# Optimization experiments

Measured on AMD Instinct MI355X. Metric: run time of the kernel, lower is better.

The kernel has to match this reference:

```python
import jax, jax.numpy as jnp
import numpy as np

H, HD, C = 16, 64, 64            # num_heads, head_dim, mini_batch_size
BASE_LR = 1.0
EPS = 1e-6                        # ttt LN eps (ln_fwd / ln_fused_l2_bwd)


def _l2norm(x):
    return x / jnp.maximum(jnp.linalg.norm(x, axis=-1, keepdims=True), 1e-12)


def _ln_fwd(x, g, b):
    mu = x.mean(-1, keepdims=True)
    var = x.var(-1, keepdims=True)
    return g * ((x - mu) * jax.lax.rsqrt(var + EPS)) + b


def _ln_l2_bwd(x, tgt, g, b):
    # gradient of ||LN(x)*g+b - tgt||^2 / 2 wrt x
    D = x.shape[-1]
    mu = x.mean(-1, keepdims=True)
    var = x.var(-1, keepdims=True)
    std = jnp.sqrt(var + EPS)
    xh = (x - mu) / std
    gout = (g * xh + b) - tgt
    gxh = gout * g
    return (D * gxh - gxh.sum(-1, keepdims=True) - xh * (gxh * xh).sum(-1, keepdims=True)) / (D * std)


def setup_inputs() -> dict:
    key = jax.random.key(0)
    ks = jax.random.split(key, 12)
    B, L, D = 4, 8192, 1024
    std = 0.02
    return {
        'hidden_states': jax.random.normal(ks[0], (B, L, D), jnp.float32),
        'wq_w': jax.random.normal(ks[1], (D, D), jnp.float32) * std,
        'wq_b': jnp.zeros((D,), jnp.float32),
        'wk_w': jax.random.normal(ks[2], (D, D), jnp.float32) * std,
        'wk_b': jnp.zeros((D,), jnp.float32),
        'wv_w': jax.random.normal(ks[3], (D, D), jnp.float32) * std,
        'wv_b': jnp.zeros((D,), jnp.float32),
        'wo_w': jax.random.normal(ks[4], (D, D), jnp.float32) * std,
        'wo_b': jnp.zeros((D,), jnp.float32),
        'ttt_norm_weight': jnp.ones((H, HD), jnp.float32),
        'ttt_norm_bias': jnp.zeros((H, HD), jnp.float32),
        'ttt_lr_weight': jax.random.normal(ks[5], (H, 1, D), jnp.float32) * std,
        'ttt_lr_bias': jnp.zeros((H, 1), jnp.float32),
        'W1': jax.random.normal(ks[6], (H, HD, HD), jnp.float32) * std,
        'b1': jnp.zeros((H, 1, HD), jnp.float32),
        'post_norm_w': jnp.ones((D,), jnp.float32),
        'post_norm_b': jnp.zeros((D,), jnp.float32),
    }


def _forward(hidden_states, wq_w, wq_b, wk_w, wk_b, wv_w, wv_b, wo_w, wo_b,
             ttt_norm_weight, ttt_norm_bias, ttt_lr_weight, ttt_lr_bias,
             W1, b1, post_norm_w, post_norm_b):
    B, L, D = hidden_states.shape
    NC = L // C
    XQ = (hidden_states @ wq_w.T + wq_b).reshape(B, L, H, HD)
    XK = (hidden_states @ wk_w.T + wk_b).reshape(B, L, H, HD)
    XV = (hidden_states @ wv_w.T + wv_b).reshape(B, L, H, HD)
    XQ = _l2norm(XQ)
    XK = _l2norm(XK)
    # ln_reconstruction_target (uses sample std, ddof=1, eps=1e-5 on std)
    d = XV - XK
    mu = d.mean(-1, keepdims=True)
    sd = d.std(-1, keepdims=True, ddof=1)
    XV = ttt_norm_weight[None, None] * ((d - mu) / (sd + 1e-5)) + ttt_norm_bias[None, None] + XK
    # reshape to mini-batches: [B,H,NC,C,HD]
    Xmb = hidden_states.reshape(B, NC, C, D)
    to_mb = lambda t: t.transpose(0, 2, 1, 3).reshape(B, H, NC, C, HD)
    XQ, XK, XV = to_mb(XQ), to_mb(XK), to_mb(XV)
    # eta: sigmoid lr gate per token, row-broadcast over mini-batch
    ttt_lr = jax.nn.sigmoid(jnp.einsum('bnkc,hdc->bhnkd', Xmb, ttt_lr_weight)
                            + ttt_lr_bias.reshape(1, H, 1, 1, 1))     # [B,H,NC,C,1]
    eta = jnp.swapaxes(ttt_lr, -1, -2) * (BASE_LR / HD / C)           # [B,H,NC,1,C]
    mask = jnp.tril(jnp.ones((C, C), hidden_states.dtype))
    g = ttt_norm_weight[None, :, None, :]
    bta = ttt_norm_bias[None, :, None, :]
    W0 = jnp.broadcast_to(W1[None], (B, H, HD, HD))
    b0 = jnp.broadcast_to(b1[None], (B, H, 1, HD))

    def step(carry, xs):
        W, bvec = carry
        xq, xk, xv, eta_row = xs                      # eta_row: [B,H,1,C]
        Z1 = xk @ W + bvec                            # [B,H,C,HD]
        grad = _ln_l2_bwd(Z1, xv - xk, g, bta)        # [B,H,C,HD]
        Attn = mask * jnp.einsum('bhid,bhjd->bhij', xq, xk)   # [B,H,C,C]
        eta_full = jnp.broadcast_to(eta_row, Attn.shape)      # [B,H,C,C]
        b1_bar = bvec - (mask * eta_full) @ grad              # [B,H,C,HD]
        Z1_bar = xq @ W - (eta_full * Attn) @ grad + b1_bar
        last_eta = eta_full[..., -1, :, None]                 # [B,H,C,1]
        W_new = W - jnp.einsum('bhcd,bhce->bhde', last_eta * xk, grad)
        b_new = bvec - (last_eta * grad).sum(-2, keepdims=True)
        out = xq + _ln_fwd(Z1_bar, g, bta)
        return (W_new, b_new), out

    xs = (jnp.moveaxis(XQ, 2, 0), jnp.moveaxis(XK, 2, 0),
          jnp.moveaxis(XV, 2, 0), jnp.moveaxis(eta, 2, 0))
    _, outs = jax.lax.scan(step, (W0, b0), xs)        # outs: [NC,B,H,C,HD]
    y = jnp.moveaxis(outs, 0, 2).reshape(B, H, L, HD).transpose(0, 2, 1, 3).reshape(B, L, D)
    # post LayerNorm (eps=1e-6) + output projection
    mu2 = y.mean(-1, keepdims=True)
    var2 = y.var(-1, keepdims=True)
    y = post_norm_w * ((y - mu2) * jax.lax.rsqrt(var2 + 1e-6)) + post_norm_b
    return y @ wo_w.T + wo_b


def reference(hidden_states, wq_w, wq_b, wk_w, wk_b, wv_w, wv_b, wo_w, wo_b,
              ttt_norm_weight, ttt_norm_bias, ttt_lr_weight, ttt_lr_bias,
              W1, b1, post_norm_w, post_norm_b):
    return _forward(hidden_states, wq_w, wq_b, wk_w, wk_b, wv_w, wv_b, wo_w, wo_b,
                    ttt_norm_weight, ttt_norm_bias, ttt_lr_weight, ttt_lr_bias,
                    W1, b1, post_norm_w, post_norm_b)
```

## Files before the change

kernel.cpp:

```cpp
#include <hip/hip_runtime.h>


typedef __attribute__((ext_vector_type(8))) short short8;
typedef __attribute__((ext_vector_type(4))) float f32x4;
typedef __attribute__((ext_vector_type(4))) unsigned short us4;

__device__ __forceinline__ float bf2f(unsigned short s) {
  union { unsigned int u; float f; } c;
  c.u = ((unsigned int)s) << 16;
  return c.f;
}
__device__ __forceinline__ unsigned short f2bf(float f) {
  union { float f; unsigned int u; } c;
  c.f = f;
  unsigned int u = c.u;
  return (unsigned short)((u + 0x7FFFu + ((u >> 16) & 1u)) >> 16);
}

__device__ __forceinline__ void gload_lds16(const void* g, void* l) {
  __builtin_amdgcn_global_load_lds(
      (const __attribute__((address_space(1))) unsigned int*)g,
      (__attribute__((address_space(3))) unsigned int*)l, 16, 0, 0);
}

__device__ __forceinline__ float dpp16_sum(float x) {
  int v = __float_as_int(x);
  x += __int_as_float(__builtin_amdgcn_update_dpp(v, v, 0xB1, 0xF, 0xF, true));
  v = __float_as_int(x);
  x += __int_as_float(__builtin_amdgcn_update_dpp(v, v, 0x4E, 0xF, 0xF, true));
  v = __float_as_int(x);
  x += __int_as_float(__builtin_amdgcn_update_dpp(v, v, 0x141, 0xF, 0xF, true));
  v = __float_as_int(x);
  x += __int_as_float(__builtin_amdgcn_update_dpp(v, v, 0x140, 0xF, 0xF, true));
  return x;
}

__device__ __forceinline__ void barrier_fast() {
  __builtin_amdgcn_sched_barrier(0);
  asm volatile("s_waitcnt lgkmcnt(0)" ::: "memory");
  __builtin_amdgcn_s_barrier();
  asm volatile("" ::: "memory");
  __builtin_amdgcn_sched_barrier(0);
}
__device__ __forceinline__ void bar_nowait() {
  __builtin_amdgcn_sched_barrier(0);
  asm volatile("" ::: "memory");
  __builtin_amdgcn_s_barrier();
  asm volatile("" ::: "memory");
  __builtin_amdgcn_sched_barrier(0);
}

__global__ __launch_bounds__(256) void cvt_f32_bf16(
    const float* __restrict__ in, unsigned short* __restrict__ out, long n) {
  long i = ((long)blockIdx.x * 256 + threadIdx.x) * 4;
  if (i + 3 < n) {
    float4 v = *(const float4*)&in[i];
    us4 o = { f2bf(v.x), f2bf(v.y), f2bf(v.z), f2bf(v.w) };
    *(us4*)&out[i] = o;
  }
}

__global__ __launch_bounds__(256) void build_wcat(
    const float* __restrict__ wq, const float* __restrict__ wk,
    const float* __restrict__ wv, const float* __restrict__ lrw,
    const float* __restrict__ wqb, const float* __restrict__ wkb,
    const float* __restrict__ wvb, const float* __restrict__ lrb,
    unsigned short* __restrict__ Wcat, float* __restrict__ biasc) {
  int i = blockIdx.x * 256 + threadIdx.x;
  int row = i >> 10, col = i & 1023;
  float v;
  if (row < 1024)      v = wq[i];
  else if (row < 2048) v = wk[i - 1048576];
  else if (row < 3072) v = wv[i - 2097152];
  else if (row < 3088) v = lrw[(row - 3072) * 1024 + col];
  else                 v = 0.f;
  Wcat[i] = f2bf(v);
  if (i < 3328) {
    float bv;
    if (i < 1024)      bv = wqb[i];
    else if (i < 2048) bv = wkb[i - 1024];
    else if (i < 3072) bv = wvb[i - 2048];
    else if (i < 3088) bv = lrb[i - 3072];
    else               bv = 0.f;
    biasc[i] = bv;
  }
}

template <int WRITE_BF16>
__global__ __launch_bounds__(512, 1) void gemm256(
    const unsigned short* __restrict__ A, const unsigned short* __restrict__ B,
    const float* __restrict__ bias, void* __restrict__ Cout,
    long M, long N, long K, int NTILN, long ldc) {
  __shared__ __align__(16) unsigned short g_lds[65536];
  char* ldsc = (char*)g_lds;
  const int tid = threadIdx.x, lane = tid & 63, wid = tid >> 6;
  const int wm = wid >> 2, wn = wid & 3;
  const int l15 = lane & 15, lg = lane >> 4;

  unsigned nwg = gridDim.x, bid = blockIdx.x;
  unsigned cpx = nwg >> 3;
  unsigned swz = (bid & 7) * cpx + (bid >> 3);
  unsigned nidx = swz % (unsigned)NTILN, midx = swz / (unsigned)NTILN;
  const long m0 = (long)midx * 256, n0 = (long)nidx * 256;
  const long ldab = K * 2;

  const int srow = wid * 16 + (lane >> 2);
  const int scol = ((lane & 3) * 16) ^ (((lane >> 3) & 3) << 4);
  const int sdst = wid * 1024;
  const char* Ab = (const char*)A;
  const char* Bb = (const char*)B;

  const int acol = (lg * 16) ^ (((l15 >> 1) & 3) << 4);
  const int aro = (wm * 128 + l15) * 64 + acol;
  const int bro = 65536 + (wn * 64 + l15) * 64 + acol;

#define STG_A(tt, h, bb)                                                     \
  gload_lds16(Ab + (size_t)(m0 + (h) * 128 + srow) * ldab + (size_t)(tt) * 64 \
                  + scol,                                                     \
              ldsc + (bb) * 16384 + (h) * 8192 + sdst)
#define STG_B(tt, h, bb)                                                     \
  gload_lds16(Bb + (size_t)(n0 + (h) * 128 + srow) * ldab + (size_t)(tt) * 64 \
                  + scol,                                                     \
              ldsc + 65536 + (bb) * 16384 + (h) * 8192 + sdst)

  f32x4 acc[8][4];
#pragma unroll
  for (int m = 0; m < 8; ++m)
#pragma unroll
    for (int n = 0; n < 4; ++n) acc[m][n] = (f32x4){0.f, 0.f, 0.f, 0.f};

  const int NT = (int)(K >> 5);

#pragma unroll
  for (int tt = 0; tt < 3; ++tt) {
    STG_A(tt, 0, tt); STG_A(tt, 1, tt);
    STG_B(tt, 0, tt); STG_B(tt, 1, tt);
  }
  asm volatile("s_waitcnt vmcnt(8)" ::: "memory");
  bar_nowait();

#pragma unroll 1
  for (int t = 0; t < NT; ++t) {
    const int buf = t & 3, sb = (t + 3) & 3;
    const bool doStage = (t + 3 < NT);
    const char* ab = ldsc + buf * 16384 + aro;
    const char* bb = ldsc + buf * 16384 + bro;

    short8 av[4], bv[4];
#pragma unroll
    for (int i = 0; i < 4; ++i) av[i] = *(const short8*)(ab + i * 1024);
#pragma unroll
    for (int nf = 0; nf < 4; ++nf) bv[nf] = *(const short8*)(bb + nf * 1024);
    if (doStage) { STG_A(t + 3, 0, sb); STG_A(t + 3, 1, sb); }
    bar_nowait();
    __builtin_amdgcn_s_setprio(1);
#pragma unroll
    for (int i = 0; i < 4; ++i)
#pragma unroll
      for (int nf = 0; nf < 4; ++nf)
        acc[i][nf] = __builtin_amdgcn_mfma_f32_16x16x32_bf16(av[i], bv[nf],
                                                             acc[i][nf], 0, 0, 0);
    __builtin_amdgcn_s_setprio(0);
    bar_nowait();

#pragma unroll
    for (int i = 0; i < 4; ++i) av[i] = *(const short8*)(ab + 4096 + i * 1024);
    if (doStage) { STG_B(t + 3, 0, sb); STG_B(t + 3, 1, sb); }
    bar_nowait();
    __builtin_amdgcn_s_setprio(1);
#pragma unroll
    for (int i = 0; i < 4; ++i)
#pragma unroll
      for (int nf = 0; nf < 4; ++nf)
        acc[4 + i][nf] = __builtin_amdgcn_mfma_f32_16x16x32_bf16(
            av[i], bv[nf], acc[4 + i][nf], 0, 0, 0);
    __builtin_amdgcn_s_setprio(0);
    asm volatile("s_waitcnt vmcnt(8)" ::: "memory");
    bar_nowait();
  }
#undef STG_A
#undef STG_B

#pragma unroll
  for (int mf = 0; mf < 8; ++mf) {
    long r0 = m0 + wm * 128 + mf * 16 + lg * 4;
#pragma unroll
    for (int nf = 0; nf < 4; ++nf) {
      long c = n0 + wn * 64 + nf * 16 + l15;
      float bvv = bias ? bias[c] : 0.f;
#pragma unroll
      for (int j = 0; j < 4; ++j) {
        float v = acc[mf][nf][j] + bvv;
        if (WRITE_BF16)
          ((unsigned short*)Cout)[(r0 + j) * ldc + c] = f2bf(v);
        else
          ((float*)Cout)[(r0 + j) * ldc + c] = v;
      }
    }
  }
}

__global__ __launch_bounds__(256) void stage2(
    const unsigned short* __restrict__ QKVL, const float* __restrict__ tnw,
    const float* __restrict__ tnb, unsigned short* __restrict__ XQn,
    unsigned short* __restrict__ XKn, unsigned short* __restrict__ TGT,
    float* __restrict__ eta_buf) {
  int wid = threadIdx.x >> 6, lane = threadIdx.x & 63;
  long idx = (long)blockIdx.x * 4 + wid;
  long t = idx >> 4;
  int h = (int)(idx & 15);
  size_t base = (size_t)t * 3328;
  float q = bf2f(QKVL[base + h * 64 + lane]);
  float k = bf2f(QKVL[base + 1024 + h * 64 + lane]);
  float v = bf2f(QKVL[base + 2048 + h * 64 + lane]);
  float sq = q * q, sk = k * k;
#pragma unroll
  for (int o = 1; o < 64; o <<= 1) {
    sq += __shfl_xor(sq, o);
    sk += __shfl_xor(sk, o);
  }
  float qn = q / fmaxf(sqrtf(sq), 1e-12f);
  float kn = k / fmaxf(sqrtf(sk), 1e-12f);
  float d = v - kn;
  float s1 = d, s2 = d * d;
#pragma unroll
  for (int o = 1; o < 64; o <<= 1) {
    s1 += __shfl_xor(s1, o);
    s2 += __shfl_xor(s2, o);
  }
  float mu = s1 * 0.015625f;
  float var1 = fmaxf(s2 - 64.f * mu * mu, 0.f) * (1.f / 63.f);
  float sd = sqrtf(var1);
  float tgt = tnw[h * 64 + lane] * ((d - mu) / (sd + 1e-5f)) + tnb[h * 64 + lane];
  size_t ob = (size_t)t * 1024 + h * 64 + lane;
  XQn[ob] = f2bf(qn);
  XKn[ob] = f2bf(kn);
  TGT[ob] = f2bf(tgt);
  if (lane == 0) {
    float logit = bf2f(QKVL[base + 3072 + h]);
    float sig = 1.f / (1.f + expf(-logit));
    long bb = t >> 13, l = t & 8191;
    eta_buf[(size_t)(bb * 16 + h) * 8192 + l] = sig * (1.f / 4096.f);
  }
}

__global__ __launch_bounds__(512, 1) void ttt_scan(
    const unsigned short* __restrict__ XQ, const unsigned short* __restrict__ XK,
    const unsigned short* __restrict__ TG, const float* __restrict__ eta_buf,
    const float* __restrict__ W1, const float* __restrict__ b1,
    const float* __restrict__ tnw, const float* __restrict__ tnb,
    float* __restrict__ y) {
  const int bh = blockIdx.x;
  const int b = bh >> 4, h = bh & 15;
  const int tid = threadIdx.x;
  const int lane = tid & 63, wid = tid >> 6;
  const bool isA = wid < 4;
  const int q = wid & 3;
  const int l15 = lane & 15, lg = lane >> 4;

  __shared__ __align__(16) unsigned short xq_s[2][64 * 72];
  __shared__ __align__(16) unsigned short tg_s[2][64 * 72];
  __shared__ __align__(16) unsigned short xk_s[2][64 * 72];
  __shared__ __align__(16) unsigned short gc_s[64 * 72];
  __shared__ __align__(16) unsigned short gradT[64 * 72];
  __shared__ __align__(16) unsigned short xkTe[64 * 72];
  __shared__ __align__(16) unsigned short WT_b[2][64 * 72];
  __shared__ float eta_s[2][64];
  __shared__ float bpart[4][64];

  const size_t tokb = (size_t)b * 8192;
  const int col0 = h * 64;
  const int rr_ = q * 16 + (lane >> 3);
  const int c8_ = (lane & 7) * 8;

  short8 pA0[2], pA1[2], pB0[2];
  float peta = 0.f;
  float bstv[4], gwv[4], gbv[4];
  f32x4 Wreg[4];

  if (isA) {
#pragma unroll
    for (int n = 0; n < 4; ++n) {
      int e = n * 16 + l15;
      bstv[n] = b1[h * 64 + e];
      gwv[n] = tnw[h * 64 + e];
      gbv[n] = tnb[h * 64 + e];
    }
#pragma unroll
    for (int j = 0; j < 2; ++j) {
      size_t g = (tokb + rr_ + j * 8) * 1024 + col0 + c8_;
      pA0[j] = *(const short8*)&XQ[g];
      pA1[j] = *(const short8*)&TG[g];
    }
#pragma unroll
    for (int j = 0; j < 2; ++j) {
      int rr = rr_ + j * 8;
      *(short8*)&xq_s[0][rr * 72 + c8_] = pA0[j];
      *(short8*)&tg_s[0][rr * 72 + c8_] = pA1[j];
    }
#pragma unroll
    for (int j = 0; j < 2; ++j) {
      size_t g = (tokb + 64 + rr_ + j * 8) * 1024 + col0 + c8_;
      pA0[j] = *(const short8*)&XQ[g];
      pA1[j] = *(const short8*)&TG[g];
    }
  } else {
#pragma unroll
    for (int j = 0; j < 2; ++j)
      pB0[j] = *(const short8*)&XK[(tokb + rr_ + j * 8) * 1024 + col0 + c8_];
#pragma unroll
    for (int j = 0; j < 2; ++j)
      *(short8*)&xk_s[0][(rr_ + j * 8) * 72 + c8_] = pB0[j];
#pragma unroll
    for (int j = 0; j < 2; ++j)
      pB0[j] = *(const short8*)&XK[(tokb + 64 + rr_ + j * 8) * 1024 + col0 + c8_];
#pragma unroll
    for (int n = 0; n < 4; ++n)
#pragma unroll
      for (int jj = 0; jj < 4; ++jj) {
        int d = q * 16 + lg * 4 + jj, e = n * 16 + l15;
        float w = W1[h * 4096 + d * 64 + e];
        Wreg[n][jj] = w;
        WT_b[0][e * 72 + d] = f2bf(w);
      }
    if (wid == 4) {
      eta_s[0][lane] = eta_buf[(size_t)bh * 8192 + lane];
      peta = eta_buf[(size_t)bh * 8192 + 64 + lane];
    }
  }
  __syncthreads();

  for (int nc = 0; nc < 128; ++nc) {
    const int p = nc & 1;
    const unsigned short* WTc = WT_b[p];
    unsigned short* WTn = WT_b[p ^ 1];

    if (isA) {
      if (nc) {
#pragma unroll
        for (int n = 0; n < 4; ++n) {
          int e = n * 16 + l15;
          bstv[n] -= bpart[0][e] + bpart[1][e] + bpart[2][e] + bpart[3][e];
        }
      }
      if (nc + 1 < 128) {
#pragma unroll
        for (int j = 0; j < 2; ++j) {
          int rr = rr_ + j * 8;
          *(short8*)&xq_s[p ^ 1][rr * 72 + c8_] = pA0[j];
          *(short8*)&tg_s[p ^ 1][rr * 72 + c8_] = pA1[j];
        }
      }
      if (nc + 2 < 128) {
#pragma unroll
        for (int j = 0; j < 2; ++j) {
          size_t g = (tokb + (nc + 2) * 64 + rr_ + j * 8) * 1024 + col0 + c8_;
          pA0[j] = *(const short8*)&XQ[g];
          pA1[j] = *(const short8*)&TG[g];
        }
      }
      f32x4 accZ[4];
#pragma unroll
      for (int n = 0; n < 4; ++n)
        accZ[n] = (f32x4){bstv[n], bstv[n], bstv[n], bstv[n]};
      __builtin_amdgcn_s_setprio(1);
#pragma unroll
      for (int kk = 0; kk < 2; ++kk) {
        const int ko = kk * 32 + lg * 8;
        short8 a_xk = *(const short8*)&xk_s[p][(q * 16 + l15) * 72 + ko];
#pragma unroll
        for (int n = 0; n < 4; ++n) {
          short8 b_w = *(const short8*)&WTc[(n * 16 + l15) * 72 + ko];
          accZ[n] = __builtin_amdgcn_mfma_f32_16x16x32_bf16(a_xk, b_w, accZ[n], 0, 0, 0);
        }
      }
      __builtin_amdgcn_s_setprio(0);
      float grv[4][4];
#pragma unroll
      for (int j = 0; j < 4; ++j) {
        const int r = q * 16 + lg * 4 + j;
        float z[4], s1 = 0.f, s2 = 0.f;
#pragma unroll
        for (int n = 0; n < 4; ++n) {
          z[n] = accZ[n][j];
          s1 += z[n];
          s2 += z[n] * z[n];
        }
        s1 = dpp16_sum(s1);
        s2 = dpp16_sum(s2);
        float mu = s1 * 0.015625f;
        float var = s2 * 0.015625f - mu * mu;
        float rstd = rsqrtf(var + 1e-6f);
        float xh[4], gx[4], s3 = 0.f, s4 = 0.f;
#pragma unroll
        for (int n = 0; n < 4; ++n) {
          xh[n] = (z[n] - mu) * rstd;
          float tg = bf2f(tg_s[p][r * 72 + n * 16 + l15]);
          float go = gwv[n] * xh[n] + gbv[n] - tg;
          gx[n] = go * gwv[n];
          s3 += gx[n];
          s4 += gx[n] * xh[n];
        }
        s3 = dpp16_sum(s3);
        s4 = dpp16_sum(s4);
#pragma unroll
        for (int n = 0; n < 4; ++n)
          grv[n][j] = (64.f * gx[n] - s3 - xh[n] * s4) * rstd * 0.015625f;
      }
#pragma unroll
      for (int n = 0; n < 4; ++n) {
        us4 pk = {f2bf(grv[n][0]), f2bf(grv[n][1]), f2bf(grv[n][2]),
                  f2bf(grv[n][3])};
        *(us4*)&gradT[(n * 16 + l15) * 72 + q * 16 + lg * 4] = pk;
      }
    } else {
      if (nc + 1 < 128) {
#pragma unroll
        for (int j = 0; j < 2; ++j)
          *(short8*)&xk_s[p ^ 1][(rr_ + j * 8) * 72 + c8_] = pB0[j];
        if (wid == 4) eta_s[p ^ 1][lane] = peta;
      }
      if (nc + 2 < 128) {
#pragma unroll
        for (int j = 0; j < 2; ++j)
          pB0[j] = *(const short8*)
              &XK[(tokb + (nc + 2) * 64 + rr_ + j * 8) * 1024 + col0 + c8_];
        if (wid == 4) peta = eta_buf[(size_t)bh * 8192 + (nc + 2) * 64 + lane];
      }
#pragma unroll
      for (int it = 0; it < 4; ++it) {
        int c0 = q * 16 + it * 4;
        us4 pk;
#pragma unroll
        for (int u = 0; u < 4; ++u)
          pk[u] = f2bf(-eta_s[p][c0 + u] * bf2f(xk_s[p][(c0 + u) * 72 + lane]));
        *(us4*)&xkTe[lane * 72 + c0] = pk;
      }
      f32x4 accA[4];
#pragma unroll
      for (int n = 0; n < 4; ++n) accA[n] = (f32x4){0.f, 0.f, 0.f, 0.f};
      __builtin_amdgcn_s_setprio(1);
#pragma unroll
      for (int kk = 0; kk < 2; ++kk) {
        const int ko = kk * 32 + lg * 8;
        short8 a_xq = *(const short8*)&xq_s[p][(q * 16 + l15) * 72 + ko];
#pragma unroll
        for (int n = 0; n < 4; ++n) {
          short8 b_k = *(const short8*)&xk_s[p][(n * 16 + l15) * 72 + ko];
          accA[n] = __builtin_amdgcn_mfma_f32_16x16x32_bf16(a_xq, b_k, accA[n], 0, 0, 0);
        }
      }
      __builtin_amdgcn_s_setprio(0);
#pragma unroll
      for (int j = 0; j < 4; ++j) {
        const int r = q * 16 + lg * 4 + j;
#pragma unroll
        for (int n = 0; n < 4; ++n) {
          int cj = n * 16 + l15;
          float v = (cj <= r) ? (-eta_s[p][cj] * (1.f + accA[n][j])) : 0.f;
          gc_s[r * 72 + cj] = f2bf(v);
        }
      }
    }
    barrier_fast();

    if (isA) {
      f32x4 accZb[4];
#pragma unroll
      for (int n = 0; n < 4; ++n)
        accZb[n] = (f32x4){bstv[n], bstv[n], bstv[n], bstv[n]};
      __builtin_amdgcn_s_setprio(1);
#pragma unroll
      for (int kk = 0; kk < 2; ++kk) {
        const int ko = kk * 32 + lg * 8;
        short8 a_xq = *(const short8*)&xq_s[p][(q * 16 + l15) * 72 + ko];
        short8 a_gc = *(const short8*)&gc_s[(q * 16 + l15) * 72 + ko];
#pragma unroll
        for (int n = 0; n < 4; ++n) {
          short8 b_w = *(const short8*)&WTc[(n * 16 + l15) * 72 + ko];
          short8 b_g = *(const short8*)&gradT[(n * 16 + l15) * 72 + ko];
          accZb[n] = __builtin_amdgcn_mfma_f32_16x16x32_bf16(a_xq, b_w, accZb[n], 0, 0, 0);
          accZb[n] = __builtin_amdgcn_mfma_f32_16x16x32_bf16(a_gc, b_g, accZb[n], 0, 0, 0);
        }
      }
      __builtin_amdgcn_s_setprio(0);
#pragma unroll
      for (int j = 0; j < 4; ++j) {
        const int r = q * 16 + lg * 4 + j;
        float z[4], s1 = 0.f, s2 = 0.f;
#pragma unroll
        for (int n = 0; n < 4; ++n) {
          z[n] = accZb[n][j];
          s1 += z[n];
          s2 += z[n] * z[n];
        }
        s1 = dpp16_sum(s1);
        s2 = dpp16_sum(s2);
        float mu = s1 * 0.015625f;
        float var = s2 * 0.015625f - mu * mu;
        float rstd = rsqrtf(var + 1e-6f);
        size_t gbase = (tokb + nc * 64 + r) * 1024 + col0;
#pragma unroll
        for (int n = 0; n < 4; ++n) {
          int e = n * 16 + l15;
          float ov = bf2f(xq_s[p][r * 72 + e]) + gwv[n] * ((z[n] - mu) * rstd) + gbv[n];
          y[gbase + e] = ov;
        }
      }
    } else {
      f32x4 accW[4];
#pragma unroll
      for (int n = 0; n < 4; ++n) accW[n] = Wreg[n];
      __builtin_amdgcn_s_setprio(1);
#pragma unroll
      for (int kk = 0; kk < 2; ++kk) {
        const int ko = kk * 32 + lg * 8;
        short8 a_ke = *(const short8*)&xkTe[(q * 16 + l15) * 72 + ko];
#pragma unroll
        for (int n = 0; n < 4; ++n) {
          short8 b_g = *(const short8*)&gradT[(n * 16 + l15) * 72 + ko];
          accW[n] = __builtin_amdgcn_mfma_f32_16x16x32_bf16(a_ke, b_g, accW[n], 0, 0, 0);
        }
      }
      __builtin_amdgcn_s_setprio(0);
#pragma unroll
      for (int n = 0; n < 4; ++n) {
        Wreg[n] = accW[n];
        us4 pk = {f2bf(accW[n][0]), f2bf(accW[n][1]), f2bf(accW[n][2]),
                  f2bf(accW[n][3])};
        *(us4*)&WTn[(n * 16 + l15) * 72 + q * 16 + lg * 4] = pk;
      }
      {
        float s = 0.f;
#pragma unroll
        for (int it = 0; it < 4; ++it) {
          us4 gv = *(const us4*)&gradT[lane * 72 + q * 16 + it * 4];
#pragma unroll
          for (int u = 0; u < 4; ++u)
            s += eta_s[p][q * 16 + it * 4 + u] * bf2f(gv[u]);
        }
        bpart[q][lane] = s;
      }
    }
    barrier_fast();
  }
}

__global__ __launch_bounds__(256) void postnorm(
    const float* __restrict__ yv, const float* __restrict__ pw,
    const float* __restrict__ pb, unsigned short* __restrict__ yn) {
  int t = blockIdx.x;
  int tid = threadIdx.x, lane = tid & 63, wid = tid >> 6;
  const float* row = yv + (size_t)t * 1024;
  float4 v = *(const float4*)&row[tid * 4];
  float s1 = v.x + v.y + v.z + v.w;
  float s2 = v.x * v.x + v.y * v.y + v.z * v.z + v.w * v.w;
#pragma unroll
  for (int o = 1; o < 64; o <<= 1) {
    s1 += __shfl_xor(s1, o);
    s2 += __shfl_xor(s2, o);
  }
  __shared__ float r1[4], r2[4];
  if (lane == 0) {
    r1[wid] = s1;
    r2[wid] = s2;
  }
  __syncthreads();
  s1 = r1[0] + r1[1] + r1[2] + r1[3];
  s2 = r2[0] + r2[1] + r2[2] + r2[3];
  float mu = s1 * (1.f / 1024.f);
  float var = s2 * (1.f / 1024.f) - mu * mu;
  float rstd = rsqrtf(var + 1e-6f);
  int c = tid * 4;
  us4 o4 = {f2bf(pw[c] * ((v.x - mu) * rstd) + pb[c]),
            f2bf(pw[c + 1] * ((v.y - mu) * rstd) + pb[c + 1]),
            f2bf(pw[c + 2] * ((v.z - mu) * rstd) + pb[c + 2]),
            f2bf(pw[c + 3] * ((v.w - mu) * rstd) + pb[c + 3])};
  *(us4*)&yn[(size_t)t * 1024 + c] = o4;
}

extern "C" void kernel_launch(void* const* d_in, const int* in_sizes, int n_in,
                              void* d_out, int out_size, void* d_ws,
                              size_t ws_size, hipStream_t stream) {
  const float* hs  = (const float*)d_in[0];
  const float* wqw = (const float*)d_in[1];
  const float* wqb = (const float*)d_in[2];
  const float* wkw = (const float*)d_in[3];
  const float* wkb = (const float*)d_in[4];
  const float* wvw = (const float*)d_in[5];
  const float* wvb = (const float*)d_in[6];
  const float* wow = (const float*)d_in[7];
  const float* wob = (const float*)d_in[8];
  const float* tnw = (const float*)d_in[9];
  const float* tnb = (const float*)d_in[10];
  const float* lrw = (const float*)d_in[11];
  const float* lrb = (const float*)d_in[12];
  const float* W1  = (const float*)d_in[13];
  const float* b1  = (const float*)d_in[14];
  const float* pnw = (const float*)d_in[15];
  const float* pnb = (const float*)d_in[16];

  const size_t OFF_WCAT  = 67108864;
  const size_t OFF_BIASC = OFF_WCAT + 6815744;
  const size_t OFF_WOBF  = OFF_BIASC + 16384;
  const size_t OFF_QKVL  = OFF_WOBF + 2097152;
  const size_t OFF_XK    = OFF_QKVL + 218103808;
  const size_t OFF_TGT   = OFF_XK + 67108864;
  const size_t OFF_ETA   = OFF_TGT + 67108864;
  const size_t NEEDED    = OFF_ETA + 2097152;
  if (ws_size < NEEDED) return;

  char* ws = (char*)d_ws;
  unsigned short* hs_bf = (unsigned short*)ws;
  unsigned short* XQn   = (unsigned short*)ws;
  unsigned short* Wcat  = (unsigned short*)(ws + OFF_WCAT);
  float* biasc          = (float*)(ws + OFF_BIASC);
  unsigned short* wo_bf = (unsigned short*)(ws + OFF_WOBF);
  unsigned short* QKVL  = (unsigned short*)(ws + OFF_QKVL);
  float* yv             = (float*)(ws + OFF_QKVL);
  unsigned short* ynorm = (unsigned short*)(ws + OFF_QKVL + 134217728);
  unsigned short* XKn   = (unsigned short*)(ws + OFF_XK);
  unsigned short* TGT   = (unsigned short*)(ws + OFF_TGT);
  float* eta_buf        = (float*)(ws + OFF_ETA);

  cvt_f32_bf16<<<32768, 256, 0, stream>>>(hs, hs_bf, 33554432L);
  build_wcat<<<13312, 256, 0, stream>>>(wqw, wkw, wvw, lrw, wqb, wkb, wvb, lrb,
                                        Wcat, biasc);
  cvt_f32_bf16<<<1024, 256, 0, stream>>>(wow, wo_bf, 1048576L);
  gemm256<1><<<1664, 512, 0, stream>>>(hs_bf, Wcat, biasc, QKVL,
                                       32768L, 3328L, 1024L, 13, 3328L);
  stage2<<<131072, 256, 0, stream>>>(QKVL, tnw, tnb, XQn, XKn, TGT, eta_buf);
  ttt_scan<<<64, 512, 0, stream>>>(XQn, XKn, TGT, eta_buf, W1, b1, tnw, tnb, yv);
  postnorm<<<32768, 256, 0, stream>>>(yv, pnw, pnb, ynorm);
  gemm256<0><<<512, 512, 0, stream>>>(ynorm, wo_bf, wob, d_out,
                                      32768L, 1024L, 1024L, 4, 1024L);
}
```

Before: 956.2 us.

## Fuse QKV normalization and eta into TTT scan, store y as bf16

Removes the stage2 kernel and folds the L2 norms, the target LayerNorm and the sigmoid eta into the scan's prefetch/commit path, which now reads QKVL directly. The scan output and postnorm input become bf16 instead of fp32, halving that traffic. The LN backward is reworked algebraically to use precomputed gamma sums, the bias-gradient partial moves to the A waves, and LDS fragment loads are hoisted ahead of the MFMAs. In exchange the 64 serial scan blocks carry extra ALU work per chunk, which could lengthen the critical path, and y loses precision.

```diff
diff --git a/kernel.cpp b/kernel.cpp
--- a/kernel.cpp
+++ b/kernel.cpp
@@ -2,6 +2,7 @@
 
 
 typedef __attribute__((ext_vector_type(8))) short short8;
+typedef __attribute__((ext_vector_type(4))) short short4v;
 typedef __attribute__((ext_vector_type(4))) float f32x4;
 typedef __attribute__((ext_vector_type(4))) unsigned short us4;
 
@@ -32,6 +33,12 @@
   x += __int_as_float(__builtin_amdgcn_update_dpp(v, v, 0x141, 0xF, 0xF, true));
   v = __float_as_int(x);
   x += __int_as_float(__builtin_amdgcn_update_dpp(v, v, 0x140, 0xF, 0xF, true));
+  return x;
+}
+__device__ __forceinline__ float sum8(float x) {
+  x += __shfl_xor(x, 1);
+  x += __shfl_xor(x, 2);
+  x += __shfl_xor(x, 4);
   return x;
 }
 
@@ -114,11 +121,11 @@
   const int aro = (wm * 128 + l15) * 64 + acol;
   const int bro = 65536 + (wn * 64 + l15) * 64 + acol;
 
-#define STG_A(tt, h, bb)                                                     \
+#define STG_A(tt, h, bb)                                                      \
   gload_lds16(Ab + (size_t)(m0 + (h) * 128 + srow) * ldab + (size_t)(tt) * 64 \
                   + scol,                                                     \
               ldsc + (bb) * 16384 + (h) * 8192 + sdst)
-#define STG_B(tt, h, bb)                                                     \
+#define STG_B(tt, h, bb)                                                      \
   gload_lds16(Bb + (size_t)(n0 + (h) * 128 + srow) * ldab + (size_t)(tt) * 64 \
                   + scol,                                                     \
               ldsc + 65536 + (bb) * 16384 + (h) * 8192 + sdst)
@@ -200,56 +207,10 @@
   }
 }
 
-__global__ __launch_bounds__(256) void stage2(
-    const unsigned short* __restrict__ QKVL, const float* __restrict__ tnw,
-    const float* __restrict__ tnb, unsigned short* __restrict__ XQn,
-    unsigned short* __restrict__ XKn, unsigned short* __restrict__ TGT,
-    float* __restrict__ eta_buf) {
-  int wid = threadIdx.x >> 6, lane = threadIdx.x & 63;
-  long idx = (long)blockIdx.x * 4 + wid;
-  long t = idx >> 4;
-  int h = (int)(idx & 15);
-  size_t base = (size_t)t * 3328;
-  float q = bf2f(QKVL[base + h * 64 + lane]);
-  float k = bf2f(QKVL[base + 1024 + h * 64 + lane]);
-  float v = bf2f(QKVL[base + 2048 + h * 64 + lane]);
-  float sq = q * q, sk = k * k;
-#pragma unroll
-  for (int o = 1; o < 64; o <<= 1) {
-    sq += __shfl_xor(sq, o);
-    sk += __shfl_xor(sk, o);
-  }
-  float qn = q / fmaxf(sqrtf(sq), 1e-12f);
-  float kn = k / fmaxf(sqrtf(sk), 1e-12f);
-  float d = v - kn;
-  float s1 = d, s2 = d * d;
-#pragma unroll
-  for (int o = 1; o < 64; o <<= 1) {
-    s1 += __shfl_xor(s1, o);
-    s2 += __shfl_xor(s2, o);
-  }
-  float mu = s1 * 0.015625f;
-  float var1 = fmaxf(s2 - 64.f * mu * mu, 0.f) * (1.f / 63.f);
-  float sd = sqrtf(var1);
-  float tgt = tnw[h * 64 + lane] * ((d - mu) / (sd + 1e-5f)) + tnb[h * 64 + lane];
-  size_t ob = (size_t)t * 1024 + h * 64 + lane;
-  XQn[ob] = f2bf(qn);
-  XKn[ob] = f2bf(kn);
-  TGT[ob] = f2bf(tgt);
-  if (lane == 0) {
-    float logit = bf2f(QKVL[base + 3072 + h]);
-    float sig = 1.f / (1.f + expf(-logit));
-    long bb = t >> 13, l = t & 8191;
-    eta_buf[(size_t)(bb * 16 + h) * 8192 + l] = sig * (1.f / 4096.f);
-  }
-}
-
 __global__ __launch_bounds__(512, 1) void ttt_scan(
-    const unsigned short* __restrict__ XQ, const unsigned short* __restrict__ XK,
-    const unsigned short* __restrict__ TG, const float* __restrict__ eta_buf,
-    const float* __restrict__ W1, const float* __restrict__ b1,
-    const float* __restrict__ tnw, const float* __restrict__ tnb,
-    float* __restrict__ y) {
+    const unsigned short* __restrict__ QKVL, const float* __restrict__ W1,
+    const float* __restrict__ b1, const float* __restrict__ tnw,
+    const float* __restrict__ tnb, unsigned short* __restrict__ y) {
   const int bh = blockIdx.x;
   const int b = bh >> 4, h = bh & 15;
   const int tid = threadIdx.x;
@@ -263,57 +224,113 @@
   __shared__ __align__(16) unsigned short xk_s[2][64 * 72];
   __shared__ __align__(16) unsigned short gc_s[64 * 72];
   __shared__ __align__(16) unsigned short gradT[64 * 72];
-  __shared__ __align__(16) unsigned short xkTe[64 * 72];
   __shared__ __align__(16) unsigned short WT_b[2][64 * 72];
+  __shared__ __align__(16) unsigned short xkTe[64 * 68];
   __shared__ float eta_s[2][64];
   __shared__ float bpart[4][64];
 
   const size_t tokb = (size_t)b * 8192;
   const int col0 = h * 64;
+  const size_t qcol = (size_t)h * 64;
+  const size_t kcol = 1024 + (size_t)h * 64;
+  const size_t vcol = 2048 + (size_t)h * 64;
+  const size_t lcol = 3072 + (size_t)h;
   const int rr_ = q * 16 + (lane >> 3);
   const int c8_ = (lane & 7) * 8;
 
-  short8 pA0[2], pA1[2], pB0[2];
-  float peta = 0.f;
-  float bstv[4], gwv[4], gbv[4];
+  short8 pQ[2], pK[2], pV[2];
+  unsigned short plr = 0;
+  float bstv[4], gwv[4], gbv[4], P0 = 0.f;
+  float twB[8], tbB[8];
   f32x4 Wreg[4];
 
+  auto commitA = [&](int bb) {
+#pragma unroll
+    for (int j = 0; j < 2; ++j) {
+      float f[8], s = 0.f;
+#pragma unroll
+      for (int u = 0; u < 8; ++u) {
+        f[u] = bf2f((unsigned short)pQ[j][u]);
+        s += f[u] * f[u];
+      }
+      s = sum8(s);
+      float rn = 1.f / fmaxf(sqrtf(s), 1e-12f);
+      short8 o;
+#pragma unroll
+      for (int u = 0; u < 8; ++u) o[u] = (short)f2bf(f[u] * rn);
+      *(short8*)&xq_s[bb][(rr_ + j * 8) * 72 + c8_] = o;
+    }
+  };
+  auto commitB = [&](int bb) {
+#pragma unroll
+    for (int j = 0; j < 2; ++j) {
+      float kf[8], vf[8];
+      float sk2 = 0.f, sk1 = 0.f, sv1 = 0.f, sv2 = 0.f, svk = 0.f;
+#pragma unroll
+      for (int u = 0; u < 8; ++u) {
+        kf[u] = bf2f((unsigned short)pK[j][u]);
+        vf[u] = bf2f((unsigned short)pV[j][u]);
+        sk2 += kf[u] * kf[u];
+        sk1 += kf[u];
+        sv1 += vf[u];
+        sv2 += vf[u] * vf[u];
+        svk += vf[u] * kf[u];
+      }
+      sk2 = sum8(sk2); sk1 = sum8(sk1); sv1 = sum8(sv1);
+      sv2 = sum8(sv2); svk = sum8(svk);
+      float rsk = 1.f / fmaxf(sqrtf(sk2), 1e-12f);
+      float mu = (sv1 - rsk * sk1) * 0.015625f;
+      float d2 = sv2 - 2.f * rsk * svk + rsk * rsk * sk2;
+      float var1 = fmaxf(d2 - 64.f * mu * mu, 0.f) * (1.f / 63.f);
+      float rs = 1.f / (sqrtf(var1) + 1e-5f);
+      short8 ok, ot;
+#pragma unroll
+      for (int u = 0; u < 8; ++u) {
+        float kn = kf[u] * rsk;
+        float tg = twB[u] * ((vf[u] - kn - mu) * rs) + tbB[u];
+        ok[u] = (short)f2bf(kn);
+        ot[u] = (short)f2bf(tg);
+      }
+      *(short8*)&xk_s[bb][(rr_ + j * 8) * 72 + c8_] = ok;
+      *(short8*)&tg_s[bb][(rr_ + j * 8) * 72 + c8_] = ot;
+    }
+    if (wid == 4) {
+      float lgt = bf2f(plr);
+      eta_s[bb][lane] = (1.f / 4096.f) / (1.f + __expf(-lgt));
+    }
+  };
+
   if (isA) {
+#pragma unroll
+    for (int j = 0; j < 2; ++j)
+      pQ[j] = *(const short8*)&QKVL[(tokb + rr_ + j * 8) * 3328 + qcol + c8_];
 #pragma unroll
     for (int n = 0; n < 4; ++n) {
       int e = n * 16 + l15;
       bstv[n] = b1[h * 64 + e];
       gwv[n] = tnw[h * 64 + e];
       gbv[n] = tnb[h * 64 + e];
-    }
+      P0 += gwv[n] * gwv[n];
+    }
+    P0 = dpp16_sum(P0);
+    commitA(0);
+#pragma unroll
+    for (int j = 0; j < 2; ++j)
+      pQ[j] = *(const short8*)&QKVL[(tokb + 64 + rr_ + j * 8) * 3328 + qcol + c8_];
+  } else {
 #pragma unroll
     for (int j = 0; j < 2; ++j) {
-      size_t g = (tokb + rr_ + j * 8) * 1024 + col0 + c8_;
-      pA0[j] = *(const short8*)&XQ[g];
-      pA1[j] = *(const short8*)&TG[g];
-    }
-#pragma unroll
-    for (int j = 0; j < 2; ++j) {
-      int rr = rr_ + j * 8;
-      *(short8*)&xq_s[0][rr * 72 + c8_] = pA0[j];
-      *(short8*)&tg_s[0][rr * 72 + c8_] = pA1[j];
-    }
-#pragma unroll
-    for (int j = 0; j < 2; ++j) {
-      size_t g = (tokb + 64 + rr_ + j * 8) * 1024 + col0 + c8_;
-      pA0[j] = *(const short8*)&XQ[g];
-      pA1[j] = *(const short8*)&TG[g];
-    }
-  } else {
-#pragma unroll
-    for (int j = 0; j < 2; ++j)
-      pB0[j] = *(const short8*)&XK[(tokb + rr_ + j * 8) * 1024 + col0 + c8_];
-#pragma unroll
-    for (int j = 0; j < 2; ++j)
-      *(short8*)&xk_s[0][(rr_ + j * 8) * 72 + c8_] = pB0[j];
-#pragma unroll
-    for (int j = 0; j < 2; ++j)
-      pB0[j] = *(const short8*)&XK[(tokb + 64 + rr_ + j * 8) * 1024 + col0 + c8_];
+      pK[j] = *(const short8*)&QKVL[(tokb + rr_ + j * 8) * 3328 + kcol + c8_];
+      pV[j] = *(const short8*)&QKVL[(tokb + rr_ + j * 8) * 3328 + vcol + c8_];
+    }
+    if (wid == 4) plr = QKVL[(tokb + lane) * 3328 + lcol];
+#pragma unroll
+    for (int u = 0; u < 4; ++u) {
+      twB[u] = tnw[h * 64 + c8_ + u];
+      twB[u + 4] = tnw[h * 64 + c8_ + 4 + u];
+      tbB[u] = tnb[h * 64 + c8_ + u];
+      tbB[u + 4] = tnb[h * 64 + c8_ + 4 + u];
+    }
 #pragma unroll
     for (int n = 0; n < 4; ++n)
 #pragma unroll
@@ -323,10 +340,13 @@
         Wreg[n][jj] = w;
         WT_b[0][e * 72 + d] = f2bf(w);
       }
-    if (wid == 4) {
-      eta_s[0][lane] = eta_buf[(size_t)bh * 8192 + lane];
-      peta = eta_buf[(size_t)bh * 8192 + 64 + lane];
-    }
+    commitB(0);
+#pragma unroll
+    for (int j = 0; j < 2; ++j) {
+      pK[j] = *(const short8*)&QKVL[(tokb + 64 + rr_ + j * 8) * 3328 + kcol + c8_];
+      pV[j] = *(const short8*)&QKVL[(tokb + 64 + rr_ + j * 8) * 3328 + vcol + c8_];
+    }
+    if (wid == 4) plr = QKVL[(tokb + 64 + lane) * 3328 + lcol];
   }
   __syncthreads();
 
@@ -336,97 +356,121 @@
     unsigned short* WTn = WT_b[p ^ 1];
 
     if (isA) {
-      if (nc) {
-#pragma unroll
-        for (int n = 0; n < 4; ++n) {
-          int e = n * 16 + l15;
-          bstv[n] -= bpart[0][e] + bpart[1][e] + bpart[2][e] + bpart[3][e];
-        }
-      }
-      if (nc + 1 < 128) {
-#pragma unroll
-        for (int j = 0; j < 2; ++j) {
-          int rr = rr_ + j * 8;
-          *(short8*)&xq_s[p ^ 1][rr * 72 + c8_] = pA0[j];
-          *(short8*)&tg_s[p ^ 1][rr * 72 + c8_] = pA1[j];
-        }
-      }
-      if (nc + 2 < 128) {
-#pragma unroll
-        for (int j = 0; j < 2; ++j) {
-          size_t g = (tokb + (nc + 2) * 64 + rr_ + j * 8) * 1024 + col0 + c8_;
-          pA0[j] = *(const short8*)&XQ[g];
-          pA1[j] = *(const short8*)&TG[g];
-        }
-      }
+      short8 a_xk[2], b_w[2][4];
+#pragma unroll
+      for (int kk = 0; kk < 2; ++kk) {
+        const int ko = kk * 32 + lg * 8;
+        a_xk[kk] = *(const short8*)&xk_s[p][(q * 16 + l15) * 72 + ko];
+#pragma unroll
+        for (int n = 0; n < 4; ++n)
+          b_w[kk][n] = *(const short8*)&WTc[(n * 16 + l15) * 72 + ko];
+      }
+      float tval[4][4];
+#pragma unroll
+      for (int j = 0; j < 4; ++j) {
+        const int r = q * 16 + lg * 4 + j;
+#pragma unroll
+        for (int n = 0; n < 4; ++n)
+          tval[j][n] = bf2f(tg_s[p][r * 72 + n * 16 + l15]);
+      }
+      float etar[4];
+#pragma unroll
+      for (int j = 0; j < 4; ++j) etar[j] = eta_s[p][q * 16 + lg * 4 + j];
+
       f32x4 accZ[4];
 #pragma unroll
       for (int n = 0; n < 4; ++n)
         accZ[n] = (f32x4){bstv[n], bstv[n], bstv[n], bstv[n]};
       __builtin_amdgcn_s_setprio(1);
 #pragma unroll
-      for (int kk = 0; kk < 2; ++kk) {
-        const int ko = kk * 32 + lg * 8;
-        short8 a_xk = *(const short8*)&xk_s[p][(q * 16 + l15) * 72 + ko];
-#pragma unroll
-        for (int n = 0; n < 4; ++n) {
-          short8 b_w = *(const short8*)&WTc[(n * 16 + l15) * 72 + ko];
-          accZ[n] = __builtin_amdgcn_mfma_f32_16x16x32_bf16(a_xk, b_w, accZ[n], 0, 0, 0);
-        }
-      }
+      for (int kk = 0; kk < 2; ++kk)
+#pragma unroll
+        for (int n = 0; n < 4; ++n)
+          accZ[n] = __builtin_amdgcn_mfma_f32_16x16x32_bf16(a_xk[kk], b_w[kk][n],
+                                                            accZ[n], 0, 0, 0);
       __builtin_amdgcn_s_setprio(0);
+
+      if (nc + 1 < 128) commitA(p ^ 1);
+      if (nc + 2 < 128) {
+#pragma unroll
+        for (int j = 0; j < 2; ++j)
+          pQ[j] = *(const short8*)
+              &QKVL[(tokb + (nc + 2) * 64 + rr_ + j * 8) * 3328 + qcol + c8_];
+      }
+
       float grv[4][4];
+      float bl[4] = {0.f, 0.f, 0.f, 0.f};
 #pragma unroll
       for (int j = 0; j < 4; ++j) {
-        const int r = q * 16 + lg * 4 + j;
-        float z[4], s1 = 0.f, s2 = 0.f;
+        float z[4], cn[4];
+        float a1 = 0.f, a2 = 0.f, p1 = 0.f, p2 = 0.f, q0 = 0.f, q1 = 0.f;
 #pragma unroll
         for (int n = 0; n < 4; ++n) {
           z[n] = accZ[n][j];
-          s1 += z[n];
-          s2 += z[n] * z[n];
-        }
-        s1 = dpp16_sum(s1);
-        s2 = dpp16_sum(s2);
-        float mu = s1 * 0.015625f;
-        float var = s2 * 0.015625f - mu * mu;
+          float g = gwv[n];
+          float g2 = g * g;
+          cn[n] = g * (gbv[n] - tval[j][n]);
+          a1 += z[n];
+          a2 += z[n] * z[n];
+          p1 += g2 * z[n];
+          p2 += g2 * z[n] * z[n];
+          q0 += cn[n];
+          q1 += cn[n] * z[n];
+        }
+        a1 = dpp16_sum(a1);
+        a2 = dpp16_sum(a2);
+        p1 = dpp16_sum(p1);
+        p2 = dpp16_sum(p2);
+        q0 = dpp16_sum(q0);
+        q1 = dpp16_sum(q1);
+        float mu = a1 * 0.015625f;
+        float var = a2 * 0.015625f - mu * mu;
         float rstd = rsqrtf(var + 1e-6f);
-        float xh[4], gx[4], s3 = 0.f, s4 = 0.f;
+        float S3 = rstd * (p1 - mu * P0) + q0;
+        float S4 = rstd * rstd * (p2 - 2.f * mu * p1 + mu * mu * P0) +
+                   rstd * (q1 - mu * q0);
+        float rs64 = rstd * 0.015625f;
 #pragma unroll
         for (int n = 0; n < 4; ++n) {
-          xh[n] = (z[n] - mu) * rstd;
-          float tg = bf2f(tg_s[p][r * 72 + n * 16 + l15]);
-          float go = gwv[n] * xh[n] + gbv[n] - tg;
-          gx[n] = go * gwv[n];
-          s3 += gx[n];
-          s4 += gx[n] * xh[n];
-        }
-        s3 = dpp16_sum(s3);
-        s4 = dpp16_sum(s4);
-#pragma unroll
-        for (int n = 0; n < 4; ++n)
-          grv[n][j] = (64.f * gx[n] - s3 - xh[n] * s4) * rstd * 0.015625f;
+          float xh = (z[n] - mu) * rstd;
+          float gx = gwv[n] * gwv[n] * xh + cn[n];
+          float gr = (64.f * gx - S3 - xh * S4) * rs64;
+          grv[n][j] = gr;
+          bl[n] += etar[j] * gr;
+        }
       }
 #pragma unroll
       for (int n = 0; n < 4; ++n) {
         us4 pk = {f2bf(grv[n][0]), f2bf(grv[n][1]), f2bf(grv[n][2]),
                   f2bf(grv[n][3])};
         *(us4*)&gradT[(n * 16 + l15) * 72 + q * 16 + lg * 4] = pk;
+        float s = bl[n];
+        s += __shfl_xor(s, 16);
+        s += __shfl_xor(s, 32);
+        if (lg == 0) bpart[q][n * 16 + l15] = s;
       }
     } else {
-      if (nc + 1 < 128) {
-#pragma unroll
-        for (int j = 0; j < 2; ++j)
-          *(short8*)&xk_s[p ^ 1][(rr_ + j * 8) * 72 + c8_] = pB0[j];
-        if (wid == 4) eta_s[p ^ 1][lane] = peta;
-      }
-      if (nc + 2 < 128) {
-#pragma unroll
-        for (int j = 0; j < 2; ++j)
-          pB0[j] = *(const short8*)
-              &XK[(tokb + (nc + 2) * 64 + rr_ + j * 8) * 1024 + col0 + c8_];
-        if (wid == 4) peta = eta_buf[(size_t)bh * 8192 + (nc + 2) * 64 + lane];
-      }
+      short8 a_xq[2], b_k[2][4];
+#pragma unroll
+      for (int kk = 0; kk < 2; ++kk) {
+        const int ko = kk * 32 + lg * 8;
+        a_xq[kk] = *(const short8*)&xq_s[p][(q * 16 + l15) * 72 + ko];
+#pragma unroll
+        for (int n = 0; n < 4; ++n)
+          b_k[kk][n] = *(const short8*)&xk_s[p][(n * 16 + l15) * 72 + ko];
+      }
+      f32x4 accA[4];
+#pragma unroll
+      for (int n = 0; n < 4; ++n) accA[n] = (f32x4){0.f, 0.f, 0.f, 0.f};
+      __builtin_amdgcn_s_setprio(1);
+#pragma unroll
+      for (int kk = 0; kk < 2; ++kk)
+#pragma unroll
+        for (int n = 0; n < 4; ++n)
+          accA[n] = __builtin_amdgcn_mfma_f32_16x16x32_bf16(a_xq[kk], b_k[kk][n],
+                                                            accA[n], 0, 0, 0);
+      __builtin_amdgcn_s_setprio(0);
+
 #pragma unroll
       for (int it = 0; it < 4; ++it) {
         int c0 = q * 16 + it * 4;
@@ -434,23 +478,21 @@
 #pragma unroll
         for (int u = 0; u < 4; ++u)
           pk[u] = f2bf(-eta_s[p][c0 + u] * bf2f(xk_s[p][(c0 + u) * 72 + lane]));
-        *(us4*)&xkTe[lane * 72 + c0] = pk;
-      }
-      f32x4 accA[4];
-#pragma unroll
-      for (int n = 0; n < 4; ++n) accA[n] = (f32x4){0.f, 0.f, 0.f, 0.f};
-      __builtin_amdgcn_s_setprio(1);
-#pragma unroll
-      for (int kk = 0; kk < 2; ++kk) {
-        const int ko = kk * 32 + lg * 8;
-        short8 a_xq = *(const short8*)&xq_s[p][(q * 16 + l15) * 72 + ko];
-#pragma unroll
-        for (int n = 0; n < 4; ++n) {
-          short8 b_k = *(const short8*)&xk_s[p][(n * 16 + l15) * 72 + ko];
-          accA[n] = __builtin_amdgcn_mfma_f32_16x16x32_bf16(a_xq, b_k, accA[n], 0, 0, 0);
-        }
-      }
-      __builtin_amdgcn_s_setprio(0);
+        *(us4*)&xkTe[lane * 68 + c0] = pk;
+      }
+
+      if (nc + 1 < 128) commitB(p ^ 1);
+      if (nc + 2 < 128) {
+#pragma unroll
+        for (int j = 0; j < 2; ++j) {
+          pK[j] = *(const short8*)
+              &QKVL[(tokb + (nc + 2) * 64 + rr_ + j * 8) * 3328 + kcol + c8_];
+          pV[j] = *(const short8*)
+              &QKVL[(tokb + (nc + 2) * 64 + rr_ + j * 8) * 3328 + vcol + c8_];
+        }
+        if (wid == 4) plr = QKVL[(tokb + (nc + 2) * 64 + lane) * 3328 + lcol];
+      }
+
 #pragma unroll
       for (int j = 0; j < 4; ++j) {
         const int r = q * 16 + lg * 4 + j;
@@ -465,25 +507,40 @@
     barrier_fast();
 
     if (isA) {
+      short8 a_xq[2], a_gc[2], b_w[2][4], b_g[2][4];
+#pragma unroll
+      for (int kk = 0; kk < 2; ++kk) {
+        const int ko = kk * 32 + lg * 8;
+        a_xq[kk] = *(const short8*)&xq_s[p][(q * 16 + l15) * 72 + ko];
+        a_gc[kk] = *(const short8*)&gc_s[(q * 16 + l15) * 72 + ko];
+#pragma unroll
+        for (int n = 0; n < 4; ++n) {
+          b_w[kk][n] = *(const short8*)&WTc[(n * 16 + l15) * 72 + ko];
+          b_g[kk][n] = *(const short8*)&gradT[(n * 16 + l15) * 72 + ko];
+        }
+      }
       f32x4 accZb[4];
 #pragma unroll
       for (int n = 0; n < 4; ++n)
         accZb[n] = (f32x4){bstv[n], bstv[n], bstv[n], bstv[n]};
       __builtin_amdgcn_s_setprio(1);
 #pragma unroll
-      for (int kk = 0; kk < 2; ++kk) {
-        const int ko = kk * 32 + lg * 8;
-        short8 a_xq = *(const short8*)&xq_s[p][(q * 16 + l15) * 72 + ko];
-        short8 a_gc = *(const short8*)&gc_s[(q * 16 + l15) * 72 + ko];
+      for (int kk = 0; kk < 2; ++kk)
 #pragma unroll
         for (int n = 0; n < 4; ++n) {
-          short8 b_w = *(const short8*)&WTc[(n * 16 + l15) * 72 + ko];
-          short8 b_g = *(const short8*)&gradT[(n * 16 + l15) * 72 + ko];
-          accZb[n] = __builtin_amdgcn_mfma_f32_16x16x32_bf16(a_xq, b_w, accZb[n], 0, 0, 0);
-          accZb[n] = __builtin_amdgcn_mfma_f32_16x16x32_bf16(a_gc, b_g, accZb[n], 0, 0, 0);
-        }
-      }
+          accZb[n] = __builtin_amdgcn_mfma_f32_16x16x32_bf16(a_xq[kk], b_w[kk][n],
+                                                             accZb[n], 0, 0, 0);
+          accZb[n] = __builtin_amdgcn_mfma_f32_16x16x32_bf16(a_gc[kk], b_g[kk][n],
+                                                             accZb[n], 0, 0, 0);
+        }
       __builtin_amdgcn_s_setprio(0);
+
+#pragma unroll
+      for (int n = 0; n < 4; ++n) {
+        int e = n * 16 + l15;
+        bstv[n] -= bpart[0][e] + bpart[1][e] + bpart[2][e] + bpart[3][e];
+      }
+
 #pragma unroll
       for (int j = 0; j < 4; ++j) {
         const int r = q * 16 + lg * 4 + j;
@@ -504,24 +561,31 @@
         for (int n = 0; n < 4; ++n) {
           int e = n * 16 + l15;
           float ov = bf2f(xq_s[p][r * 72 + e]) + gwv[n] * ((z[n] - mu) * rstd) + gbv[n];
-          y[gbase + e] = ov;
+          y[gbase + e] = f2bf(ov);
         }
       }
     } else {
+      short8 a_ke[2], b_g[2][4];
+#pragma unroll
+      for (int kk = 0; kk < 2; ++kk) {
+        const int ko = kk * 32 + lg * 8;
+        short4v lo = *(const short4v*)&xkTe[(q * 16 + l15) * 68 + ko];
+        short4v hi = *(const short4v*)&xkTe[(q * 16 + l15) * 68 + ko + 4];
+        a_ke[kk] = (short8){lo[0], lo[1], lo[2], lo[3], hi[0], hi[1], hi[2], hi[3]};
+#pragma unroll
+        for (int n = 0; n < 4; ++n)
+          b_g[kk][n] = *(const short8*)&gradT[(n * 16 + l15) * 72 + ko];
+      }
       f32x4 accW[4];
 #pragma unroll
       for (int n = 0; n < 4; ++n) accW[n] = Wreg[n];
       __builtin_amdgcn_s_setprio(1);
 #pragma unroll
-      for (int kk = 0; kk < 2; ++kk) {
-        const int ko = kk * 32 + lg * 8;
-        short8 a_ke = *(const short8*)&xkTe[(q * 16 + l15) * 72 + ko];
-#pragma unroll
-        for (int n = 0; n < 4; ++n) {
-          short8 b_g = *(const short8*)&gradT[(n * 16 + l15) * 72 + ko];
-          accW[n] = __builtin_amdgcn_mfma_f32_16x16x32_bf16(a_ke, b_g, accW[n], 0, 0, 0);
-        }
-      }
+      for (int kk = 0; kk < 2; ++kk)
+#pragma unroll
+        for (int n = 0; n < 4; ++n)
+          accW[n] = __builtin_amdgcn_mfma_f32_16x16x32_bf16(a_ke[kk], b_g[kk][n],
+                                                            accW[n], 0, 0, 0);
       __builtin_amdgcn_s_setprio(0);
 #pragma unroll
       for (int n = 0; n < 4; ++n) {
@@ -530,31 +594,25 @@
                   f2bf(accW[n][3])};
         *(us4*)&WTn[(n * 16 + l15) * 72 + q * 16 + lg * 4] = pk;
       }
-      {
-        float s = 0.f;
-#pragma unroll
-        for (int it = 0; it < 4; ++it) {
-          us4 gv = *(const us4*)&gradT[lane * 72 + q * 16 + it * 4];
-#pragma unroll
-          for (int u = 0; u < 4; ++u)
-            s += eta_s[p][q * 16 + it * 4 + u] * bf2f(gv[u]);
-        }
-        bpart[q][lane] = s;
-      }
     }
     barrier_fast();
   }
 }
 
 __global__ __launch_bounds__(256) void postnorm(
-    const float* __restrict__ yv, const float* __restrict__ pw,
+    const unsigned short* __restrict__ yv, const float* __restrict__ pw,
     const float* __restrict__ pb, unsigned short* __restrict__ yn) {
   int t = blockIdx.x;
   int tid = threadIdx.x, lane = tid & 63, wid = tid >> 6;
-  const float* row = yv + (size_t)t * 1024;
-  float4 v = *(const float4*)&row[tid * 4];
-  float s1 = v.x + v.y + v.z + v.w;
-  float s2 = v.x * v.x + v.y * v.y + v.z * v.z + v.w * v.w;
+  us4 v4 = *(const us4*)&yv[(size_t)t * 1024 + tid * 4];
+  float v[4];
+  float s1 = 0.f, s2 = 0.f;
+#pragma unroll
+  for (int u = 0; u < 4; ++u) {
+    v[u] = bf2f(v4[u]);
+    s1 += v[u];
+    s2 += v[u] * v[u];
+  }
 #pragma unroll
   for (int o = 1; o < 64; o <<= 1) {
     s1 += __shfl_xor(s1, o);
@@ -572,10 +630,10 @@
   float var = s2 * (1.f / 1024.f) - mu * mu;
   float rstd = rsqrtf(var + 1e-6f);
   int c = tid * 4;
-  us4 o4 = {f2bf(pw[c] * ((v.x - mu) * rstd) + pb[c]),
-            f2bf(pw[c + 1] * ((v.y - mu) * rstd) + pb[c + 1]),
-            f2bf(pw[c + 2] * ((v.z - mu) * rstd) + pb[c + 2]),
-            f2bf(pw[c + 3] * ((v.w - mu) * rstd) + pb[c + 3])};
+  us4 o4;
+#pragma unroll
+  for (int u = 0; u < 4; ++u)
+    o4[u] = f2bf(pw[c + u] * ((v[u] - mu) * rstd) + pb[c + u]);
   *(us4*)&yn[(size_t)t * 1024 + c] = o4;
 }
 
@@ -604,24 +662,18 @@
   const size_t OFF_BIASC = OFF_WCAT + 6815744;
   const size_t OFF_WOBF  = OFF_BIASC + 16384;
   const size_t OFF_QKVL  = OFF_WOBF + 2097152;
-  const size_t OFF_XK    = OFF_QKVL + 218103808;
-  const size_t OFF_TGT   = OFF_XK + 67108864;
-  const size_t OFF_ETA   = OFF_TGT + 67108864;
-  const size_t NEEDED    = OFF_ETA + 2097152;
+  const size_t OFF_YN    = OFF_QKVL + 218103808;
+  const size_t NEEDED    = OFF_YN + 67108864;
   if (ws_size < NEEDED) return;
 
   char* ws = (char*)d_ws;
   unsigned short* hs_bf = (unsigned short*)ws;
-  unsigned short* XQn   = (unsigned short*)ws;
+  unsigned short* ybf   = (unsigned short*)ws;
   unsigned short* Wcat  = (unsigned short*)(ws + OFF_WCAT);
   float* biasc          = (float*)(ws + OFF_BIASC);
   unsigned short* wo_bf = (unsigned short*)(ws + OFF_WOBF);
   unsigned short* QKVL  = (unsigned short*)(ws + OFF_QKVL);
-  float* yv             = (float*)(ws + OFF_QKVL);
-  unsigned short* ynorm = (unsigned short*)(ws + OFF_QKVL + 134217728);
-  unsigned short* XKn   = (unsigned short*)(ws + OFF_XK);
-  unsigned short* TGT   = (unsigned short*)(ws + OFF_TGT);
-  float* eta_buf        = (float*)(ws + OFF_ETA);
+  unsigned short* ynorm = (unsigned short*)(ws + OFF_YN);
 
   cvt_f32_bf16<<<32768, 256, 0, stream>>>(hs, hs_bf, 33554432L);
   build_wcat<<<13312, 256, 0, stream>>>(wqw, wkw, wvw, lrw, wqb, wkb, wvb, lrb,
@@ -629,9 +681,8 @@
   cvt_f32_bf16<<<1024, 256, 0, stream>>>(wow, wo_bf, 1048576L);
   gemm256<1><<<1664, 512, 0, stream>>>(hs_bf, Wcat, biasc, QKVL,
                                        32768L, 3328L, 1024L, 13, 3328L);
-  stage2<<<131072, 256, 0, stream>>>(QKVL, tnw, tnb, XQn, XKn, TGT, eta_buf);
-  ttt_scan<<<64, 512, 0, stream>>>(XQn, XKn, TGT, eta_buf, W1, b1, tnw, tnb, yv);
-  postnorm<<<32768, 256, 0, stream>>>(yv, pnw, pnb, ynorm);
+  ttt_scan<<<64, 512, 0, stream>>>(QKVL, W1, b1, tnw, tnb, ybf);
+  postnorm<<<32768, 256, 0, stream>>>(ybf, pnw, pnb, ynorm);
   gemm256<0><<<512, 512, 0, stream>>>(ynorm, wo_bf, wob, d_out,
                                       32768L, 1024L, 1024L, 4, 1024L);
 }
```

Result: slower. 994.9 us (+4.1%).
